# Optimization experiments

Hardware: AMD Instinct MI355X
Metric: run time of the kernel (lower is better)

The kernel has to match this reference:

```python
import jax, jax.numpy as jnp
import numpy as np

B, T, C = 8, 1024, 2048
N_HEAD = 16
HEAD = C // N_HEAD  # 128


def setup_inputs() -> dict:
    key = jax.random.key(0)
    k1, k2, k3 = jax.random.split(key, 3)
    scale = 0.02
    x = jax.random.normal(k1, (B, T, C), dtype=jnp.float32)
    W_attn = jax.random.normal(k2, (C, 3 * C), dtype=jnp.float32) * scale
    b_attn = jnp.zeros((3 * C,), dtype=jnp.float32)
    W_proj = jax.random.normal(k3, (C, C), dtype=jnp.float32) * scale
    b_proj = jnp.zeros((C,), dtype=jnp.float32)
    return {"x": x, "W_attn": W_attn, "b_attn": b_attn, "W_proj": W_proj, "b_proj": b_proj}


def reference(x, W_attn, b_attn, W_proj, b_proj):
    Bq, Tq, Cq = x.shape
    qkv = x @ W_attn + b_attn                       # [B,T,3C]
    q, k, v = jnp.split(qkv, 3, axis=2)             # each [B,T,C]
    def heads(t):
        return t.reshape(Bq, Tq, N_HEAD, HEAD).transpose(0, 2, 1, 3)  # [B,H,T,D]
    q, k, v = heads(q), heads(k), heads(v)
    scores = jnp.einsum('bhqd,bhkd->bhqk', q, k) / jnp.sqrt(jnp.float32(HEAD))
    causal = jnp.tril(jnp.ones((Tq, Tq), dtype=bool))
    scores = jnp.where(causal, scores, jnp.float32(-1e9))
    attn = jax.nn.softmax(scores, axis=-1)          # [B,H,T,T]
    y = jnp.einsum('bhqk,bhkd->bhqd', attn, v)      # [B,H,T,D]
    y = y.transpose(0, 2, 1, 3).reshape(Bq, Tq, Cq) # [B,T,C]
    return y @ W_proj + b_proj
```

## Files before the change

### kernel.cpp

```cpp
#include <hip/hip_runtime.h>
#include <hip/hip_bf16.h>


typedef unsigned short u16;
typedef __bf16 bf16x8 __attribute__((ext_vector_type(8)));
typedef float f32x4 __attribute__((ext_vector_type(4)));

#define B_ 8
#define T_ 1024
#define C_ 2048
#define NH 16
#define HD 128
#define BH (B_*NH)

__device__ __forceinline__ u16 f2b(float f){
  __bf16 h = (__bf16)f; return __builtin_bit_cast(u16, h);
}
__device__ __forceinline__ unsigned pk2(float x, float y){
  return (unsigned)f2b(x) | ((unsigned)f2b(y) << 16);
}
__device__ __forceinline__ bf16x8 ldfrag(const u16* p){
  uint4 u = *(const uint4*)p; return __builtin_bit_cast(bf16x8, u);
}
__device__ __forceinline__ void glds16(const u16* g, const u16* l){
  __builtin_amdgcn_global_load_lds(
      (const __attribute__((address_space(1))) void*)g,
      (__attribute__((address_space(3))) void*)l, 16, 0, 0);
}
__device__ __forceinline__ void sbar(){
  __builtin_amdgcn_sched_barrier(0);
  __builtin_amdgcn_s_barrier();
  __builtin_amdgcn_sched_barrier(0);
}

__global__ __launch_bounds__(256) void cvt_bf16(
    const float4* __restrict__ in, ushort4* __restrict__ outp, int n4)
{
  int i = blockIdx.x*256 + threadIdx.x;
  const int stride = gridDim.x*256;
  for (; i < n4; i += stride){
    float4 f = in[i];
    ushort4 o; o.x = f2b(f.x); o.y = f2b(f.y); o.z = f2b(f.z); o.w = f2b(f.w);
    outp[i] = o;
  }
}

__global__ __launch_bounds__(256) void transpose_cvt(
    const float* __restrict__ in, u16* __restrict__ outp, int R, int C)
{
  __shared__ u16 tile[64][65];
  const int t = threadIdx.x;
  const int r0 = blockIdx.y * 64, c0 = blockIdx.x * 64;
#pragma unroll
  for (int ii = 0; ii < 16; ++ii){
    int idx = t + ii*256; int r = idx >> 6, c = idx & 63;
    tile[r][c] = f2b(in[(size_t)(r0 + r)*C + c0 + c]);
  }
  __syncthreads();
#pragma unroll
  for (int ii = 0; ii < 16; ++ii){
    int idx = t + ii*256; int r = idx >> 6, c = idx & 63;
    outp[(size_t)(c0 + r)*R + r0 + c] = tile[c][r];
  }
}

__device__ __forceinline__ void qkv_epilogue(
    const f32x4 acc[4][4], const float* bias, int bx, int by,
    int wm, int wn, int lq, int ln,
    u16* qb, u16* kb, u16* vb)
{
  const int tensor = bx >> 4, h = bx & 15, b = by >> 3, t0 = (by & 7)*128;
  u16* tb = tensor==0 ? qb : (tensor==1 ? kb : vb);
  u16* op = tb + ((size_t)(b*NH + h)*T_ + t0)*HD;
#pragma unroll
  for (int j=0;j<4;j++){
    const float bv = bias[bx*128 + wn*64 + j*16 + ln];
    const int n = wn*64 + j*16 + ln;
#pragma unroll
    for (int i=0;i<4;i++){
      const int m0 = wm*64 + i*16 + lq*4;
#pragma unroll
      for (int r=0;r<4;r++)
        op[(size_t)(m0 + r)*HD + n] = f2b(acc[i][j][r] + bv);
    }
  }
}

__global__ __launch_bounds__(512,2) void gemm_qkv_8p(
    const u16* __restrict__ Xb, const u16* __restrict__ Wt,
    const float* __restrict__ bias,
    u16* __restrict__ qb, u16* __restrict__ kb, u16* __restrict__ vb)
{
  __shared__ u16 lds[2][2][256*64];
  const int t = threadIdx.x;
  const int lane = t & 63, wid = t >> 6;
  const int lq = lane >> 4, ln = lane & 15;
  const int wm = wid >> 2, wn = wid & 3;

  const int bid0 = blockIdx.x;
  const int bid = (bid0 & 7)*96 + (bid0 >> 3);
  const int bx = bid % 24, by = bid / 24;

  const int rl  = (wid << 4) + (lane >> 3);
  const int sw0 = (lane & 7) ^ (rl & 7);
  const u16* Ag = Xb + ((size_t)(by*256) + rl)*2048;
  const u16* Bg = Wt + ((size_t)(bx*256) + rl)*2048;
  const size_t q0off = (size_t)sw0*8;
  const size_t q1off = (size_t)8*2048 + (size_t)sw0*8;

#define STAGE(buf_, op_, h_, T_) do { \
    const u16* s_ = (op_ ? Bg : Ag) + (size_t)(h_)*(128*2048) + (size_t)(T_)*64; \
    const u16* d_ = &lds[buf_][op_][(((h_)*128) + (wid<<4))*64]; \
    glds16(s_ + q0off, d_); \
    glds16(s_ + q1off, d_ + 8*64); \
  } while(0)

  const int swr0 = (0*4 + lq) ^ (ln & 7);
  const int swr1 = (1*4 + lq) ^ (ln & 7);

  const f32x4 fz = {0.f,0.f,0.f,0.f};
  f32x4 acc[8][4];
#pragma unroll
  for (int f=0;f<8;f++)
#pragma unroll
    for (int g=0;g<4;g++) acc[f][g] = fz;

  STAGE(0,0,0,0); STAGE(0,0,1,0); STAGE(0,1,0,0); STAGE(0,1,1,0);
  STAGE(1,1,0,1); STAGE(1,1,1,1); STAGE(1,0,0,1);
  asm volatile("s_waitcnt vmcnt(6)" ::: "memory");
  sbar();

  for (int T = 0; T < 32; ++T){
    const int b = T & 1;
    const u16* As = lds[b][0];
    const u16* Bs = lds[b][1];
    bf16x8 a0[4][2], a4[4][2], bfr[4][2];

#pragma unroll
    for (int f=0;f<4;f++){
      a0[f][0]  = ldfrag(&As[(wm*128 + f*16 + ln)*64 + swr0*8]);
      a0[f][1]  = ldfrag(&As[(wm*128 + f*16 + ln)*64 + swr1*8]);
      bfr[f][0] = ldfrag(&Bs[(wn*64  + f*16 + ln)*64 + swr0*8]);
      bfr[f][1] = ldfrag(&Bs[(wn*64  + f*16 + ln)*64 + swr1*8]);
    }
    if (T+1 < 32) STAGE(b^1, 0, 1, T+1);
    sbar();
    __builtin_amdgcn_s_setprio(1);
#pragma unroll
    for (int f=0;f<4;f++)
#pragma unroll
      for (int g=0;g<2;g++){
        acc[f][g] = __builtin_amdgcn_mfma_f32_16x16x32_bf16(a0[f][0], bfr[g][0], acc[f][g], 0,0,0);
        acc[f][g] = __builtin_amdgcn_mfma_f32_16x16x32_bf16(a0[f][1], bfr[g][1], acc[f][g], 0,0,0);
      }
    __builtin_amdgcn_s_setprio(0);
    sbar();

#pragma unroll
    for (int f=0;f<4;f++){
      a4[f][0] = ldfrag(&As[(wm*128 + (f+4)*16 + ln)*64 + swr0*8]);
      a4[f][1] = ldfrag(&As[(wm*128 + (f+4)*16 + ln)*64 + swr1*8]);
    }
    if (T+2 < 32) STAGE(b, 1, 0, T+2);
    sbar();
    __builtin_amdgcn_s_setprio(1);
#pragma unroll
    for (int f=0;f<4;f++)
#pragma unroll
      for (int g=0;g<2;g++){
        acc[f+4][g] = __builtin_amdgcn_mfma_f32_16x16x32_bf16(a4[f][0], bfr[g][0], acc[f+4][g], 0,0,0);
        acc[f+4][g] = __builtin_amdgcn_mfma_f32_16x16x32_bf16(a4[f][1], bfr[g][1], acc[f+4][g], 0,0,0);
      }
    __builtin_amdgcn_s_setprio(0);
    sbar();

    if (T+2 < 32) STAGE(b, 1, 1, T+2);
    sbar();
    __builtin_amdgcn_s_setprio(1);
#pragma unroll
    for (int f=0;f<4;f++)
#pragma unroll
      for (int g=2;g<4;g++){
        acc[f+4][g] = __builtin_amdgcn_mfma_f32_16x16x32_bf16(a4[f][0], bfr[g][0], acc[f+4][g], 0,0,0);
        acc[f+4][g] = __builtin_amdgcn_mfma_f32_16x16x32_bf16(a4[f][1], bfr[g][1], acc[f+4][g], 0,0,0);
      }
    __builtin_amdgcn_s_setprio(0);
    sbar();

    if (T+2 < 32) STAGE(b, 0, 0, T+2);
    if (T >= 30) asm volatile("s_waitcnt vmcnt(0)" ::: "memory");
    else         asm volatile("s_waitcnt vmcnt(6)" ::: "memory");
    sbar();
    __builtin_amdgcn_s_setprio(1);
#pragma unroll
    for (int f=0;f<4;f++)
#pragma unroll
      for (int g=2;g<4;g++){
        acc[f][g] = __builtin_amdgcn_mfma_f32_16x16x32_bf16(a0[f][0], bfr[g][0], acc[f][g], 0,0,0);
        acc[f][g] = __builtin_amdgcn_mfma_f32_16x16x32_bf16(a0[f][1], bfr[g][1], acc[f][g], 0,0,0);
      }
    __builtin_amdgcn_s_setprio(0);
    sbar();
  }
#undef STAGE

  const int tensor = bx >> 3;
  u16* tb = tensor==0 ? qb : (tensor==1 ? kb : vb);
  const int m_base = by*256 + wm*128;
#pragma unroll
  for (int g=0; g<4; ++g){
    const int ncol = (bx & 7)*256 + wn*64 + g*16 + ln;
    const float bv = bias[tensor*2048 + ncol];
    const int h = ncol >> 7, d = ncol & 127;
#pragma unroll
    for (int f=0; f<8; ++f){
      const int m0 = m_base + f*16 + lq*4;
      const int bb = m0 >> 10, tt = m0 & 1023;
      u16* op = tb + ((size_t)(bb*NH + h)*T_ + tt)*HD + d;
#pragma unroll
      for (int r=0;r<4;++r)
        op[(size_t)r*HD] = f2b(acc[f][g][r] + bv);
    }
  }
}

__global__ __launch_bounds__(512,2) void gemm_proj_8p(
    const u16* __restrict__ Y, const u16* __restrict__ Wt,
    const float* __restrict__ bias, float* __restrict__ outp)
{
  __shared__ u16 lds[2][2][256*64];
  const int t = threadIdx.x;
  const int lane = t & 63, wid = t >> 6;
  const int lq = lane >> 4, ln = lane & 15;
  const int wm = wid >> 2, wn = wid & 3;

  const int bid0 = blockIdx.x;
  const int bid = (bid0 & 7)*32 + (bid0 >> 3);
  const int bx = bid & 7, by = bid >> 3;

  const int rl  = (wid << 4) + (lane >> 3);
  const int sw0 = (lane & 7) ^ (rl & 7);
  const u16* Bg = Wt + ((size_t)(bx*256) + rl)*2048;
  const size_t bq0 = (size_t)sw0*8;
  const size_t arow0 = ((size_t)(by >> 2)*16)*1024 + (size_t)(by & 3)*256 + rl;

#define STAGEP(buf_, op_, h_, Tt_) do { \
    const u16* d_ = &lds[buf_][op_][(((h_)*128) + (wid<<4))*64]; \
    if (op_){ \
      const u16* s_ = Bg + (size_t)(h_)*(128*2048) + (size_t)(Tt_)*64; \
      glds16(s_ + bq0, d_); \
      glds16(s_ + (size_t)8*2048 + bq0, d_ + 8*64); \
    } else { \
      const u16* s_ = Y + (arow0 + (size_t)((Tt_) >> 1)*1024 + (size_t)(h_)*128)*128 \
                        + ((Tt_) & 1)*64 + sw0*8; \
      glds16(s_, d_); \
      glds16(s_ + 8*128, d_ + 8*64); \
    } \
  } while(0)

  const int swr0 = (0*4 + lq) ^ (ln & 7);
  const int swr1 = (1*4 + lq) ^ (ln & 7);

  const f32x4 fz = {0.f,0.f,0.f,0.f};
  f32x4 acc[8][4];
#pragma unroll
  for (int f=0;f<8;f++)
#pragma unroll
    for (int g=0;g<4;g++) acc[f][g] = fz;

  STAGEP(0,0,0,0); STAGEP(0,0,1,0); STAGEP(0,1,0,0); STAGEP(0,1,1,0);
  STAGEP(1,1,0,1); STAGEP(1,1,1,1); STAGEP(1,0,0,1);
  asm volatile("s_waitcnt vmcnt(6)" ::: "memory");
  sbar();

  for (int T = 0; T < 32; ++T){
    const int b = T & 1;
    const u16* As = lds[b][0];
    const u16* Bs = lds[b][1];
    bf16x8 a0[4][2], a4[4][2], bfr[4][2];

#pragma unroll
    for (int f=0;f<4;f++){
      a0[f][0]  = ldfrag(&As[(wm*128 + f*16 + ln)*64 + swr0*8]);
      a0[f][1]  = ldfrag(&As[(wm*128 + f*16 + ln)*64 + swr1*8]);
      bfr[f][0] = ldfrag(&Bs[(wn*64  + f*16 + ln)*64 + swr0*8]);
      bfr[f][1] = ldfrag(&Bs[(wn*64  + f*16 + ln)*64 + swr1*8]);
    }
    if (T+1 < 32) STAGEP(b^1, 0, 1, T+1);
    sbar();
    __builtin_amdgcn_s_setprio(1);
#pragma unroll
    for (int f=0;f<4;f++)
#pragma unroll
      for (int g=0;g<2;g++){
        acc[f][g] = __builtin_amdgcn_mfma_f32_16x16x32_bf16(a0[f][0], bfr[g][0], acc[f][g], 0,0,0);
        acc[f][g] = __builtin_amdgcn_mfma_f32_16x16x32_bf16(a0[f][1], bfr[g][1], acc[f][g], 0,0,0);
      }
    __builtin_amdgcn_s_setprio(0);
    sbar();

#pragma unroll
    for (int f=0;f<4;f++){
      a4[f][0] = ldfrag(&As[(wm*128 + (f+4)*16 + ln)*64 + swr0*8]);
      a4[f][1] = ldfrag(&As[(wm*128 + (f+4)*16 + ln)*64 + swr1*8]);
    }
    if (T+2 < 32) STAGEP(b, 1, 0, T+2);
    sbar();
    __builtin_amdgcn_s_setprio(1);
#pragma unroll
    for (int f=0;f<4;f++)
#pragma unroll
      for (int g=0;g<2;g++){
        acc[f+4][g] = __builtin_amdgcn_mfma_f32_16x16x32_bf16(a4[f][0], bfr[g][0], acc[f+4][g], 0,0,0);
        acc[f+4][g] = __builtin_amdgcn_mfma_f32_16x16x32_bf16(a4[f][1], bfr[g][1], acc[f+4][g], 0,0,0);
      }
    __builtin_amdgcn_s_setprio(0);
    sbar();

    if (T+2 < 32) STAGEP(b, 1, 1, T+2);
    sbar();
    __builtin_amdgcn_s_setprio(1);
#pragma unroll
    for (int f=0;f<4;f++)
#pragma unroll
      for (int g=2;g<4;g++){
        acc[f+4][g] = __builtin_amdgcn_mfma_f32_16x16x32_bf16(a4[f][0], bfr[g][0], acc[f+4][g], 0,0,0);
        acc[f+4][g] = __builtin_amdgcn_mfma_f32_16x16x32_bf16(a4[f][1], bfr[g][1], acc[f+4][g], 0,0,0);
      }
    __builtin_amdgcn_s_setprio(0);
    sbar();

    if (T+2 < 32) STAGEP(b, 0, 0, T+2);
    if (T >= 30) asm volatile("s_waitcnt vmcnt(0)" ::: "memory");
    else         asm volatile("s_waitcnt vmcnt(6)" ::: "memory");
    sbar();
    __builtin_amdgcn_s_setprio(1);
#pragma unroll
    for (int f=0;f<4;f++)
#pragma unroll
      for (int g=2;g<4;g++){
        acc[f][g] = __builtin_amdgcn_mfma_f32_16x16x32_bf16(a0[f][0], bfr[g][0], acc[f][g], 0,0,0);
        acc[f][g] = __builtin_amdgcn_mfma_f32_16x16x32_bf16(a0[f][1], bfr[g][1], acc[f][g], 0,0,0);
      }
    __builtin_amdgcn_s_setprio(0);
    sbar();
  }
#undef STAGEP

  const int m_base = by*256 + wm*128;
#pragma unroll
  for (int g=0; g<4; ++g){
    const int ncol = bx*256 + wn*64 + g*16 + ln;
    const float bv = bias[ncol];
#pragma unroll
    for (int f=0; f<8; ++f){
      const int m0 = m_base + f*16 + lq*4;
      float* op = outp + (size_t)m0*2048 + ncol;
#pragma unroll
      for (int r=0;r<4;++r)
        op[(size_t)r*2048] = acc[f][g][r] + bv;
    }
  }
}

__global__ __launch_bounds__(256,2) void gemm_qkv_f32(
    const float* __restrict__ X, const u16* __restrict__ Wt, const float* __restrict__ bias,
    u16* __restrict__ qb, u16* __restrict__ kb, u16* __restrict__ vb)
{
  __shared__ u16 As[128*32];
  __shared__ u16 Bs[128*32];
  const int t = threadIdx.x;
  const int bx = blockIdx.x, by = blockIdx.y;
  const int lane = t & 63, wv = t >> 6;
  const int lq = lane >> 4, ln = lane & 15;
  const int wm = wv >> 1, wn = wv & 1;

  const int ar = t >> 1, ah = t & 1;
  const float* Ap = X + (size_t)(by*128 + ar)*2048 + ah*16;
  u16* AsW = &As[ar*32 + ah*16];

  const int c0 = t, c1 = 256 + t;
  const u16* Bp0 = Wt + (size_t)(bx*128 + (c0 >> 2))*2048 + (c0 & 3)*8;
  const u16* Bp1 = Wt + (size_t)(bx*128 + (c1 >> 2))*2048 + (c1 & 3)*8;
  const u16* BsW0 = &Bs[(wv*64)*8];
  const u16* BsW1 = &Bs[(256 + wv*64)*8];

  const f32x4 fz = {0.f,0.f,0.f,0.f};
  f32x4 acc[4][4];
#pragma unroll
  for (int i=0;i<4;i++)
#pragma unroll
    for (int j=0;j<4;j++) acc[i][j] = fz;

  for (int kt = 0; kt < 64; ++kt){
    float4 a0 = *(const float4*)(Ap);
    float4 a1 = *(const float4*)(Ap + 4);
    float4 a2 = *(const float4*)(Ap + 8);
    float4 a3 = *(const float4*)(Ap + 12);
    Ap += 32;
    __syncthreads();
    uint4 w0, w1;
    w0.x = pk2(a0.x,a0.y); w0.y = pk2(a0.z,a0.w);
    w0.z = pk2(a1.x,a1.y); w0.w = pk2(a1.z,a1.w);
    w1.x = pk2(a2.x,a2.y); w1.y = pk2(a2.z,a2.w);
    w1.z = pk2(a3.x,a3.y); w1.w = pk2(a3.z,a3.w);
    *(uint4*)(AsW) = w0; *(uint4*)(AsW + 8) = w1;
    glds16(Bp0, BsW0);
    glds16(Bp1, BsW1);
    Bp0 += 32; Bp1 += 32;
    __syncthreads();
    bf16x8 af[4], bf[4];
#pragma unroll
    for (int i=0;i<4;i++) af[i] = ldfrag(&As[(wm*64 + i*16 + ln)*32 + lq*8]);
#pragma unroll
    for (int j=0;j<4;j++) bf[j] = ldfrag(&Bs[(wn*64 + j*16 + ln)*32 + lq*8]);
#pragma unroll
    for (int i=0;i<4;i++)
#pragma unroll
      for (int j=0;j<4;j++)
        acc[i][j] = __builtin_amdgcn_mfma_f32_16x16x32_bf16(af[i], bf[j], acc[i][j], 0,0,0);
  }
  qkv_epilogue(acc, bias, bx, by, wm, wn, lq, ln, qb, kb, vb);
}

__global__ __launch_bounds__(256,2) void attn_fwd(
    u16* qy, const u16* __restrict__ kk, const u16* __restrict__ vv)
{
  __shared__ u16 Ks[64*128];
  __shared__ u16 Vt[128*64];
  __shared__ u16 Ps[4*32*64];
  const int qt = 7 - blockIdx.x, bh = blockIdx.y;
  const int t = threadIdx.x;
  const int lane = t & 63, wv = t >> 6;
  const int lq = lane >> 4, ln = lane & 15;

  bf16x8 qf[2][4];
#pragma unroll
  for (int i=0;i<2;i++)
#pragma unroll
    for (int kc=0;kc<4;kc++){
      int qrow = qt*128 + wv*32 + i*16 + ln;
      qf[i][kc] = ldfrag(&qy[((size_t)bh*T_ + qrow)*HD + kc*32 + lq*8]);
    }

  const f32x4 fz = {0.f,0.f,0.f,0.f};
  f32x4 o[2][8];
#pragma unroll
  for (int i=0;i<2;i++)
#pragma unroll
    for (int jd=0;jd<8;jd++) o[i][jd] = fz;
  float mi[2][4], li[2][4];
#pragma unroll
  for (int i=0;i<2;i++)
#pragma unroll
    for (int r=0;r<4;r++){ mi[i][r] = -1e30f; li[i][r] = 0.f; }

  const float scale = 0.08838834764831843f;
  const int kr = t & 63, dbase = (t >> 6)*32;
  const int nkt = 2*qt + 2;

  uint4 kreg[4];
  uint4 vreg[4];
  {
    const uint4* ksrc = (const uint4*)(kk + (size_t)bh*T_*HD);
#pragma unroll
    for (int ii=0; ii<4; ++ii) kreg[ii] = ksrc[t + ii*256];
#pragma unroll
    for (int ch=0; ch<4; ++ch)
      vreg[ch] = *(const uint4*)&vv[((size_t)bh*T_ + kr)*HD + dbase + ch*8];
  }

  for (int kt = 0; kt < nkt; ++kt){
    __syncthreads();
    uint4* kdst = (uint4*)Ks;
#pragma unroll
    for (int ii=0; ii<4; ++ii){
      const int c = t + ii*256;
      kdst[(c & ~15) | ((c & 15) ^ ((c >> 4) & 7))] = kreg[ii];
    }
#pragma unroll
    for (int ch=0; ch<4; ++ch){
      const u16* e = (const u16*)&vreg[ch];
#pragma unroll
      for (int j=0; j<8; ++j){
        const int d = dbase + ch*8 + j;
        Vt[d*64 + (kr ^ ((d & 7) << 3))] = e[j];
      }
    }
    __syncthreads();

    {
      const int ktn = (kt+1 < nkt) ? kt+1 : kt;
      const uint4* ksrc = (const uint4*)(kk + ((size_t)bh*T_ + ktn*64)*HD);
#pragma unroll
      for (int ii=0; ii<4; ++ii) kreg[ii] = ksrc[t + ii*256];
#pragma unroll
      for (int ch=0; ch<4; ++ch)
        vreg[ch] = *(const uint4*)&vv[((size_t)bh*T_ + ktn*64 + kr)*HD + dbase + ch*8];
    }

    const bool active = (kt*64) <= (qt*128 + wv*32 + 31);
    if (active){

    f32x4 s[2][4];
#pragma unroll
    for (int i=0;i<2;i++)
#pragma unroll
      for (int j=0;j<4;j++) s[i][j] = fz;
    __builtin_amdgcn_s_setprio(1);
#pragma unroll
    for (int j=0;j<4;j++){
      bf16x8 kf[4];
      const int krow = j*16 + ln;
      const int ksw = (krow & 7) << 3;
#pragma unroll
      for (int kc=0;kc<4;kc++)
        kf[kc] = ldfrag(&Ks[krow*128 + ((kc*32 + lq*8) ^ ksw)]);
#pragma unroll
      for (int i=0;i<2;i++)
#pragma unroll
        for (int kc=0;kc<4;kc++)
          s[i][j] = __builtin_amdgcn_mfma_f32_16x16x32_bf16(qf[i][kc], kf[kc], s[i][j], 0,0,0);
    }
    __builtin_amdgcn_s_setprio(0);

#pragma unroll
    for (int i=0;i<2;i++)
#pragma unroll
      for (int j=0;j<4;j++)
#pragma unroll
        for (int r=0;r<4;r++){
          int qg = qt*128 + wv*32 + i*16 + lq*4 + r;
          int kg = kt*64 + j*16 + ln;
          float sv = s[i][j][r]*scale;
          s[i][j][r] = (kg > qg) ? -1e30f : sv;
        }

    float mxv[2][4];
#pragma unroll
    for (int i=0;i<2;i++)
#pragma unroll
      for (int r=0;r<4;r++){
        float mx = fmaxf(fmaxf(s[i][0][r], s[i][1][r]), fmaxf(s[i][2][r], s[i][3][r]));
        mx = fmaxf(mx, __shfl_xor(mx, 1));
        mx = fmaxf(mx, __shfl_xor(mx, 2));
        mx = fmaxf(mx, __shfl_xor(mx, 4));
        mx = fmaxf(mx, __shfl_xor(mx, 8));
        mxv[i][r] = mx;
      }
    bool ok = true;
#pragma unroll
    for (int i=0;i<2;i++)
#pragma unroll
      for (int r=0;r<4;r++) ok = ok && (mxv[i][r] <= mi[i][r] + 8.0f);
    if (!__all((int)ok)){
#pragma unroll
      for (int i=0;i<2;i++)
#pragma unroll
        for (int r=0;r<4;r++){
          float mnew = fmaxf(mi[i][r], mxv[i][r]);
          float alpha = __expf(mi[i][r] - mnew);
          li[i][r] *= alpha;
          mi[i][r] = mnew;
#pragma unroll
          for (int jd=0;jd<8;jd++) o[i][jd][r] *= alpha;
        }
    }
#pragma unroll
    for (int i=0;i<2;i++)
#pragma unroll
      for (int r=0;r<4;r++){
        float rs = 0.f;
#pragma unroll
        for (int j=0;j<4;j++){
          float p = __expf(s[i][j][r] - mi[i][r]);
          s[i][j][r] = p; rs += p;
        }
        rs += __shfl_xor(rs, 1); rs += __shfl_xor(rs, 2);
        rs += __shfl_xor(rs, 4); rs += __shfl_xor(rs, 8);
        li[i][r] += rs;
      }

#pragma unroll
    for (int i=0;i<2;i++)
#pragma unroll
      for (int j=0;j<4;j++)
#pragma unroll
        for (int r=0;r<4;r++){
          const int rr = i*16 + lq*4 + r;
          Ps[wv*2048 + rr*64 + ((j*16 + ln) ^ ((rr & 7) << 3))] = f2b(s[i][j][r]);
        }

    bf16x8 pf[2][2];
#pragma unroll
    for (int i=0;i<2;i++){
      const int prow = i*16 + ln;
      const int psw = (prow & 7) << 3;
#pragma unroll
      for (int kc=0;kc<2;kc++)
        pf[i][kc] = ldfrag(&Ps[wv*2048 + prow*64 + ((kc*32 + lq*8) ^ psw)]);
    }
    __builtin_amdgcn_s_setprio(1);
#pragma unroll
    for (int jd=0;jd<8;jd++){
      const int vrow = jd*16 + ln;
      const int vsw = (vrow & 7) << 3;
#pragma unroll
      for (int kc=0;kc<2;kc++){
        bf16x8 vf = ldfrag(&Vt[vrow*64 + ((kc*32 + lq*8) ^ vsw)]);
#pragma unroll
        for (int i=0;i<2;i++)
          o[i][jd] = __builtin_amdgcn_mfma_f32_16x16x32_bf16(pf[i][kc], vf, o[i][jd], 0,0,0);
      }
    }
    __builtin_amdgcn_s_setprio(0);

    }
  }

#pragma unroll
  for (int i=0;i<2;i++)
#pragma unroll
    for (int r=0;r<4;r++){
      float inv = 1.f / li[i][r];
      int row = qt*128 + wv*32 + i*16 + lq*4 + r;
#pragma unroll
      for (int jd=0;jd<8;jd++)
        qy[((size_t)bh*T_ + row)*HD + jd*16 + ln] = f2b(o[i][jd][r] * inv);
    }
}

extern "C" void kernel_launch(void* const* d_in, const int* in_sizes, int n_in,
                              void* d_out, int out_size, void* d_ws, size_t ws_size,
                              hipStream_t stream)
{
  const float* x      = (const float*)d_in[0];
  const float* W_attn = (const float*)d_in[1];
  const float* b_attn = (const float*)d_in[2];
  const float* W_proj = (const float*)d_in[3];
  const float* b_proj = (const float*)d_in[4];
  float* out = (float*)d_out;

  u16* Wat = (u16*)d_ws;
  u16* Wpt = Wat + (size_t)6144*2048;
  u16* qb  = Wpt + (size_t)2048*2048;
  u16* xb  = qb  + (size_t)BH*T_*HD;
  u16* kb  = (u16*)d_out;
  u16* vb  = kb + (size_t)BH*T_*HD;

  const size_t need = ((size_t)6144*2048 + (size_t)2048*2048
                       + 2*(size_t)BH*T_*HD) * sizeof(u16);

  hipLaunchKernelGGL(transpose_cvt, dim3(96,32,1), dim3(256,1,1), 0, stream,
                     W_attn, Wat, 2048, 6144);
  hipLaunchKernelGGL(transpose_cvt, dim3(32,32,1), dim3(256,1,1), 0, stream,
                     W_proj, Wpt, 2048, 2048);
  if (ws_size >= need){
    hipLaunchKernelGGL(cvt_bf16, dim3(1024,1,1), dim3(256,1,1), 0, stream,
                       (const float4*)x, (ushort4*)xb, (B_*T_*C_)/4);
    hipLaunchKernelGGL(gemm_qkv_8p, dim3(768,1,1), dim3(512,1,1), 0, stream,
                       xb, Wat, b_attn, qb, kb, vb);
  } else {
    hipLaunchKernelGGL(gemm_qkv_f32, dim3(48,64,1), dim3(256,1,1), 0, stream,
                       x, Wat, b_attn, qb, kb, vb);
  }
  hipLaunchKernelGGL(attn_fwd, dim3(8,BH,1), dim3(256,1,1), 0, stream,
                     qb, kb, vb);
  hipLaunchKernelGGL(gemm_proj_8p, dim3(256,1,1), dim3(512,1,1), 0, stream,
                     qb, Wpt, b_proj, out);
}
```

Before: 605.7 us.

## Double-buffer K/V tiles in attention and fuse preprocessing kernels into one launch

Attention now keeps two LDS buffers for K and V tiles, alternating per key tile, so one of the two block barriers per iteration is removed and stores of the next tile can overlap other waves' compute. The two weight transpose-converts and the x bf16 conversion are merged into a single prep kernel dispatched by blockIdx.z, cutting launch overhead. The extra LDS raises per-block shared memory, which could limit occupancy.

```diff
diff --git a/kernel.cpp b/kernel.cpp
--- a/kernel.cpp
+++ b/kernel.cpp
@@ -33,23 +33,29 @@
   __builtin_amdgcn_sched_barrier(0);
 }
 
-__global__ __launch_bounds__(256) void cvt_bf16(
-    const float4* __restrict__ in, ushort4* __restrict__ outp, int n4)
-{
-  int i = blockIdx.x*256 + threadIdx.x;
-  const int stride = gridDim.x*256;
-  for (; i < n4; i += stride){
-    float4 f = in[i];
-    ushort4 o; o.x = f2b(f.x); o.y = f2b(f.y); o.z = f2b(f.z); o.w = f2b(f.w);
-    outp[i] = o;
-  }
-}
-
-__global__ __launch_bounds__(256) void transpose_cvt(
-    const float* __restrict__ in, u16* __restrict__ outp, int R, int C)
+__global__ __launch_bounds__(256) void prep(
+    const float* __restrict__ W_attn, u16* __restrict__ Wat,
+    const float* __restrict__ W_proj, u16* __restrict__ Wpt,
+    const float4* __restrict__ x4, ushort4* __restrict__ xb4, int do_cvt)
 {
   __shared__ u16 tile[64][65];
   const int t = threadIdx.x;
+  const int z = blockIdx.z;
+  if (z == 1 && blockIdx.x >= 32){
+    if (!do_cvt) return;
+    const int n4 = (B_*T_*C_)/4;
+    int i = ((blockIdx.x - 32)*32 + blockIdx.y)*256 + t;
+    const int stride = 2048*256;
+    for (; i < n4; i += stride){
+      float4 f = x4[i];
+      ushort4 o; o.x = f2b(f.x); o.y = f2b(f.y); o.z = f2b(f.z); o.w = f2b(f.w);
+      xb4[i] = o;
+    }
+    return;
+  }
+  const float* in = (z == 0) ? W_attn : W_proj;
+  u16* outp       = (z == 0) ? Wat    : Wpt;
+  const int R = 2048, C = (z == 0) ? 6144 : 2048;
   const int r0 = blockIdx.y * 64, c0 = blockIdx.x * 64;
 #pragma unroll
   for (int ii = 0; ii < 16; ++ii){
@@ -426,8 +432,8 @@
 __global__ __launch_bounds__(256,2) void attn_fwd(
     u16* qy, const u16* __restrict__ kk, const u16* __restrict__ vv)
 {
-  __shared__ u16 Ks[64*128];
-  __shared__ u16 Vt[128*64];
+  __shared__ u16 Ks[2][64*128];
+  __shared__ u16 Vt[2][128*64];
   __shared__ u16 Ps[4*32*64];
   const int qt = 7 - blockIdx.x, bh = blockIdx.y;
   const int t = threadIdx.x;
@@ -471,8 +477,8 @@
   }
 
   for (int kt = 0; kt < nkt; ++kt){
-    __syncthreads();
-    uint4* kdst = (uint4*)Ks;
+    const int b = kt & 1;
+    uint4* kdst = (uint4*)Ks[b];
 #pragma unroll
     for (int ii=0; ii<4; ++ii){
       const int c = t + ii*256;
@@ -484,11 +490,9 @@
 #pragma unroll
       for (int j=0; j<8; ++j){
         const int d = dbase + ch*8 + j;
-        Vt[d*64 + (kr ^ ((d & 7) << 3))] = e[j];
-      }
-    }
-    __syncthreads();
-
+        Vt[b][d*64 + (kr ^ ((d & 7) << 3))] = e[j];
+      }
+    }
     {
       const int ktn = (kt+1 < nkt) ? kt+1 : kt;
       const uint4* ksrc = (const uint4*)(kk + ((size_t)bh*T_ + ktn*64)*HD);
@@ -498,6 +502,7 @@
       for (int ch=0; ch<4; ++ch)
         vreg[ch] = *(const uint4*)&vv[((size_t)bh*T_ + ktn*64 + kr)*HD + dbase + ch*8];
     }
+    __syncthreads();
 
     const bool active = (kt*64) <= (qt*128 + wv*32 + 31);
     if (active){
@@ -515,7 +520,7 @@
       const int ksw = (krow & 7) << 3;
 #pragma unroll
       for (int kc=0;kc<4;kc++)
-        kf[kc] = ldfrag(&Ks[krow*128 + ((kc*32 + lq*8) ^ ksw)]);
+        kf[kc] = ldfrag(&Ks[b][krow*128 + ((kc*32 + lq*8) ^ ksw)]);
 #pragma unroll
       for (int i=0;i<2;i++)
 #pragma unroll
@@ -607,7 +612,7 @@
       const int vsw = (vrow & 7) << 3;
 #pragma unroll
       for (int kc=0;kc<2;kc++){
-        bf16x8 vf = ldfrag(&Vt[vrow*64 + ((kc*32 + lq*8) ^ vsw)]);
+        bf16x8 vf = ldfrag(&Vt[b][vrow*64 + ((kc*32 + lq*8) ^ vsw)]);
 #pragma unroll
         for (int i=0;i<2;i++)
           o[i][jd] = __builtin_amdgcn_mfma_f32_16x16x32_bf16(pf[i][kc], vf, o[i][jd], 0,0,0);
@@ -650,14 +655,12 @@
 
   const size_t need = ((size_t)6144*2048 + (size_t)2048*2048
                        + 2*(size_t)BH*T_*HD) * sizeof(u16);
-
-  hipLaunchKernelGGL(transpose_cvt, dim3(96,32,1), dim3(256,1,1), 0, stream,
-                     W_attn, Wat, 2048, 6144);
-  hipLaunchKernelGGL(transpose_cvt, dim3(32,32,1), dim3(256,1,1), 0, stream,
-                     W_proj, Wpt, 2048, 2048);
-  if (ws_size >= need){
-    hipLaunchKernelGGL(cvt_bf16, dim3(1024,1,1), dim3(256,1,1), 0, stream,
-                       (const float4*)x, (ushort4*)xb, (B_*T_*C_)/4);
+  const int big_ws = (ws_size >= need) ? 1 : 0;
+
+  hipLaunchKernelGGL(prep, dim3(96,32,2), dim3(256,1,1), 0, stream,
+                     W_attn, Wat, W_proj, Wpt,
+                     (const float4*)x, (ushort4*)xb, big_ws);
+  if (big_ws){
     hipLaunchKernelGGL(gemm_qkv_8p, dim3(768,1,1), dim3(512,1,1), 0, stream,
                        xb, Wat, b_attn, qb, kb, vb);
   } else {
```

Measured after the change: 598.3 us. Within noise of the previous version (-1.2%).
